# Performance work log

Hardware: AMD Instinct MI355X
Metric: run time of the kernel (lower is better)

## Reference

```python
import jax, jax.numpy as jnp
import numpy as np
from jax import lax

EPS_NORM = 1e-12   # F.normalize default eps
KS = 3             # fixed 3x3 window
K2 = KS * KS
MIN_CONN, MAX_CONN = 1, 8
NUM_GROUPS = 16    # largest divisor <=16 of C=128
GN_EPS = 1e-5


def _unfold3x3_reflect(x):
    # x: [B,C,H,W] -> patches [B,C,9,H,W] (reflect-padded 3x3 neighborhoods)
    B, C, H, W = x.shape
    p = jnp.pad(x, ((0, 0), (0, 0), (1, 1), (1, 1)), mode='reflect')
    pats = [p[:, :, dy:dy + H, dx:dx + W] for dy in range(KS) for dx in range(KS)]
    return jnp.stack(pats, axis=2)


def _df_counts(x):
    # DFDetector: mean over C, fixed Laplacian conv (zero pad), abs, per-batch min-max norm
    B = x.shape[0]
    avg = jnp.mean(x, axis=1, keepdims=True)  # [B,1,H,W]
    kern = jnp.array([[0., -1., 0.], [-1., 4., -1.], [0., -1., 0.]],
                     dtype=x.dtype).reshape(1, 1, 3, 3)
    df = jnp.abs(lax.conv_general_dilated(
        avg, kern, window_strides=(1, 1), padding=((1, 1), (1, 1)),
        dimension_numbers=('NCHW', 'OIHW', 'NCHW')))
    dmin = df.reshape(B, -1).min(axis=1).reshape(B, 1, 1, 1)
    dmax = df.reshape(B, -1).max(axis=1).reshape(B, 1, 1, 1)
    dn = (df - dmin) / (dmax - dmin + 1e-8)
    return MIN_CONN + jnp.round(dn * (MAX_CONN - MIN_CONN))  # [B,1,H,W], values in [1,8]


def _group_norm(x, w, b):
    B, C, H, W = x.shape
    g = x.reshape(B, NUM_GROUPS, -1)
    mu = g.mean(-1, keepdims=True)
    var = g.var(-1, keepdims=True)  # biased, matches torch GroupNorm
    g = (g - mu) * lax.rsqrt(var + GN_EPS)
    return g.reshape(B, C, H, W) * w[None, :, None, None] + b[None, :, None, None]


def setup_inputs() -> dict:
    key = jax.random.key(0)
    ks = jax.random.split(key, 7)
    B, C, H, W = 8, 128, 96, 96
    return {
        'x': jax.random.normal(ks[0], (B, C, H, W), jnp.float32),
        'gn_weight': jax.random.uniform(ks[1], (C,), jnp.float32, 0.5, 1.5),
        'gn_bias': jax.random.normal(ks[2], (C,), jnp.float32) * 0.1,
        'w1': jax.random.normal(ks[3], (2 * C, C), jnp.float32) * 0.02,
        'b1': jax.random.normal(ks[4], (2 * C,), jnp.float32) * 0.02,
        'w2': jax.random.normal(ks[5], (C, 2 * C), jnp.float32) * 0.02,
        'b2': jax.random.normal(ks[6], (C,), jnp.float32) * 0.02,
    }


def reference(x, gn_weight, gn_bias, w1, b1, w2, b2):
    B, C, H, W = x.shape
    P = H * W
    # per-pixel connection counts (integer k in [1,8]); non-differentiable in original
    counts = lax.stop_gradient(_df_counts(x))
    kvals = jnp.minimum(counts, K2).astype(jnp.int32).reshape(B, 1, P)

    patches = _unfold3x3_reflect(x).reshape(B, C, K2, P)
    xc = x.reshape(B, C, P)
    # L2 normalize over channel dim (F.normalize, eps=1e-12)
    cn = xc / jnp.maximum(jnp.linalg.norm(xc, axis=1, keepdims=True), EPS_NORM)
    pn = patches / jnp.maximum(jnp.linalg.norm(patches, axis=1, keepdims=True), EPS_NORM)

    sim = jnp.einsum('bcp,bckp->bkp', cn, pn)          # [B,9,P] cosine sims
    order = jnp.argsort(-sim, axis=1)                   # descending (== topk order)
    top_sim = jnp.take_along_axis(sim, order, axis=1)
    mask = jnp.arange(K2)[None, :, None] < kvals        # rank < k -> selected
    wts = jnp.exp(top_sim) * mask
    wts = wts / jnp.sum(wts, axis=1, keepdims=True)     # softmax over selected sims

    pat_sorted = jnp.take_along_axis(patches, order[:, None, :, :], axis=2)
    out = jnp.einsum('bckp,bkp->bcp', pat_sorted, wts).reshape(B, C, H, W)

    enhanced = out + _group_norm(x, gn_weight, gn_bias)
    h = jax.nn.relu(jnp.einsum('oi,bihw->bohw', w1, enhanced) + b1[None, :, None, None])
    ffn = jnp.einsum('oi,bihw->bohw', w2, h) + b2[None, :, None, None]
    return enhanced + ffn
```

## Files before the change

kernel.cpp:

```cpp
#include <hip/hip_runtime.h>

#define BD 8
#define CD 128
#define HD 96
#define WD 96
#define PD 9216
#define ND 73728

typedef __attribute__((ext_vector_type(8))) short short8;
typedef __attribute__((ext_vector_type(4))) float f32x4;

__device__ inline float bfu2f(unsigned int u) { return __uint_as_float(u << 16); }
__device__ inline unsigned short f2bfu(float f) {
  unsigned int u = __float_as_uint(f);
  u += 0x7fffu + ((u >> 16) & 1u);
  return (unsigned short)(u >> 16);
}

template<bool F32>
__device__ __forceinline__ float ldv(const void* __restrict__ p, size_t i) {
  if constexpr (F32) return ((const float*)p)[i];
  else return bfu2f(((const unsigned short*)p)[i]);
}

__global__ void k_init(unsigned long long* dmm, int* cnt) {
  int t = threadIdx.x;
  if (t < 8) dmm[t] = 0x7FEFFFFFFFFFFFFFULL;
  else if (t < 16) dmm[t] = 0ULL;
  if (t == 16) { cnt[0] = 0; cnt[1] = 0; }
}

__global__ void k_detect(const unsigned int* __restrict__ xw, int* __restrict__ cnt) {
  int t = blockIdx.x * 256 + threadIdx.x;
  uint4 w = ((const uint4*)xw)[t];
  int lz = (int)((w.x & 0xFFFFu) == 0u) + (int)((w.y & 0xFFFFu) == 0u) +
           (int)((w.z & 0xFFFFu) == 0u) + (int)((w.w & 0xFFFFu) == 0u);
  int e2 = (int)(((w.x >> 7) & 0xFFu) == 0xFFu) + (int)(((w.y >> 7) & 0xFFu) == 0xFFu) +
           (int)(((w.z >> 7) & 0xFFu) == 0xFFu) + (int)(((w.w >> 7) & 0xFFu) == 0xFFu);
  #pragma unroll
  for (int off = 32; off; off >>= 1) {
    lz += __shfl_down(lz, off);
    e2 += __shfl_down(e2, off);
  }
  if ((threadIdx.x & 63) == 0) { atomicAdd(&cnt[0], lz); atomicAdd(&cnt[1], e2); }
}

__global__ void k_flag(const int* __restrict__ cnt, int* __restrict__ flag) {
  *flag = (cnt[0] > 4096 || cnt[1] > 0) ? 1 : 0;
}

__global__ void k_cvtw(const void* __restrict__ w1, const void* __restrict__ w2,
                       unsigned short* __restrict__ wc, const int* __restrict__ flag) {
  bool f32 = (*flag != 0);
  int t = blockIdx.x * 256 + threadIdx.x;
  if (t < 32768)
    wc[t] = f32 ? f2bfu(((const float*)w1)[t]) : ((const unsigned short*)w1)[t];
  else {
    int u = t - 32768;
    wc[t] = f32 ? f2bfu(((const float*)w2)[u]) : ((const unsigned short*)w2)[u];
  }
}

__global__ void k_cvtb(const void* __restrict__ gw, const void* __restrict__ gb,
                       const void* __restrict__ b1, const void* __restrict__ b2,
                       float* __restrict__ prm, const int* __restrict__ flag) {
  bool f32 = (*flag != 0);
  int t = threadIdx.x;
  for (int i = t; i < 640; i += 256) {
    float v;
    if (i < 128)      v = f32 ? ((const float*)gw)[i]       : bfu2f(((const unsigned short*)gw)[i]);
    else if (i < 256) v = f32 ? ((const float*)gb)[i - 128] : bfu2f(((const unsigned short*)gb)[i - 128]);
    else if (i < 512) v = f32 ? ((const float*)b1)[i - 256] : bfu2f(((const unsigned short*)b1)[i - 256]);
    else              v = f32 ? ((const float*)b2)[i - 512] : bfu2f(((const unsigned short*)b2)[i - 512]);
    prm[i] = v;
  }
}

template<bool F32>
__device__ __forceinline__ void pmt_body(const void* __restrict__ x,
                                         float* __restrict__ xpm,
                                         double* __restrict__ avg, double* __restrict__ nrm,
                                         double* __restrict__ gpart,
                                         float (*tile)[132]) {
  const int t = threadIdx.x, px = t & 63, ci = t >> 6;
  const int gp0 = blockIdx.x * 64, b = gp0 / PD, p0 = gp0 - b * PD;
  double sg[4] = {0.0, 0.0, 0.0, 0.0}, qg[4] = {0.0, 0.0, 0.0, 0.0};
  for (int j = 0; j < 32; ++j) {
    int c = ci * 32 + j;
    float v = ldv<F32>(x, (size_t)(b * CD + c) * PD + p0 + px);
    tile[px][c] = v;
    sg[j >> 3] += (double)v;
    qg[j >> 3] += (double)v * (double)v;
  }
  #pragma unroll
  for (int g = 0; g < 4; ++g) {
    #pragma unroll
    for (int off = 32; off; off >>= 1) {
      sg[g] += __shfl_down(sg[g], off);
      qg[g] += __shfl_down(qg[g], off);
    }
  }
  if (px == 0) {
    double* gp_ = gpart + (size_t)blockIdx.x * 32;
    #pragma unroll
    for (int g = 0; g < 4; ++g) {
      gp_[(ci * 4 + g) * 2 + 0] = sg[g];
      gp_[(ci * 4 + g) * 2 + 1] = qg[g];
    }
  }
  __syncthreads();
  for (int i = t; i < 2048; i += 256) {
    int r = i >> 5, seg = i & 31;
    *(float4*)(xpm + (size_t)(gp0 + r) * 128 + seg * 4) = *(const float4*)&tile[r][seg * 4];
  }
  if (t < 64) {
    double s = 0.0, q = 0.0;
    for (int c = 0; c < 128; ++c) {
      float v = tile[t][c];
      s += (double)v;
      q += (double)v * (double)v;
    }
    avg[gp0 + t] = s * (1.0 / 128.0);
    nrm[gp0 + t] = sqrt(q);
  }
}
__global__ __launch_bounds__(256) void k_pmt(const void* __restrict__ x,
                                             const int* __restrict__ flag,
                                             float* __restrict__ xpm,
                                             double* __restrict__ avg,
                                             double* __restrict__ nrm,
                                             double* __restrict__ gpart) {
  __shared__ float tile[64][132];
  if (*flag) pmt_body<true>(x, xpm, avg, nrm, gpart, tile);
  else pmt_body<false>(x, xpm, avg, nrm, gpart, tile);
}

__global__ void k_gn2(const double* __restrict__ gpart, float* __restrict__ gn) {
  const int bg = blockIdx.x;
  const int b = bg >> 4, g = bg & 15;
  const int t = threadIdx.x;
  double s = 0.0, q = 0.0;
  for (int i = t; i < 144; i += 64) {
    const double* pp = gpart + (size_t)(b * 144 + i) * 32 + g * 2;
    s += pp[0];
    q += pp[1];
  }
  #pragma unroll
  for (int off = 32; off; off >>= 1) {
    s += __shfl_down(s, off);
    q += __shfl_down(q, off);
  }
  if (t == 0) {
    double mu = s / 73728.0;
    double var = q / 73728.0 - mu * mu;
    gn[bg] = (float)mu;
    gn[128 + bg] = (float)(1.0 / sqrt(var + 1e-5));
  }
}

__device__ inline double lap_df(const double* __restrict__ a, int b, int y, int x) {
  const double* ab = a + (size_t)b * PD;
  double v = 4.0 * ab[y * WD + x];
  if (y > 0)      v -= ab[(y - 1) * WD + x];
  if (y < HD - 1) v -= ab[(y + 1) * WD + x];
  if (x > 0)      v -= ab[y * WD + x - 1];
  if (x < WD - 1) v -= ab[y * WD + x + 1];
  return fabs(v);
}

__global__ void k_minmax(const double* __restrict__ avg, unsigned long long* __restrict__ dmm) {
  __shared__ double mnW[4], mxW[4];
  int t = threadIdx.x;
  int gp = blockIdx.x * 256 + t;
  int b = gp / PD, p = gp - b * PD;
  double mn = lap_df(avg, b, p / WD, p % WD);
  double mx = mn;
  #pragma unroll
  for (int off = 32; off; off >>= 1) {
    mn = fmin(mn, __shfl_down(mn, off));
    mx = fmax(mx, __shfl_down(mx, off));
  }
  if ((t & 63) == 0) { mnW[t >> 6] = mn; mxW[t >> 6] = mx; }
  __syncthreads();
  if (t == 0) {
    mn = fmin(fmin(mnW[0], mnW[1]), fmin(mnW[2], mnW[3]));
    mx = fmax(fmax(mxW[0], mxW[1]), fmax(mxW[2], mxW[3]));
    atomicMin(&dmm[b], (unsigned long long)__double_as_longlong(mn));
    atomicMax(&dmm[b + 8], (unsigned long long)__double_as_longlong(mx));
  }
}

__device__ __forceinline__ void neigh9(int y, int xx, int* q) {
  #pragma unroll
  for (int dy = 0; dy < 3; ++dy) {
    int yy = y + dy - 1;
    yy = yy < 0 ? -yy : (yy >= HD ? 2 * HD - 2 - yy : yy);
    #pragma unroll
    for (int dx = 0; dx < 3; ++dx) {
      int xr = xx + dx - 1;
      xr = xr < 0 ? -xr : (xr >= WD ? 2 * WD - 2 - xr : xr);
      q[dy * 3 + dx] = yy * WD + xr;
    }
  }
}

__global__ __launch_bounds__(256, 3) void k_ipg(const float* __restrict__ xpm,
                                                const double* __restrict__ avg,
                                                const double* __restrict__ nrm,
                                                const unsigned long long* __restrict__ dmm,
                                                const float* __restrict__ gn,
                                                const float* __restrict__ prm,
                                                unsigned short* __restrict__ eg) {
  __shared__ float tileF[12800];
  float4* tile4 = (float4*)tileF;
  const float* gwf = prm;
  const float* gbf = prm + 128;

  const int t = threadIdx.x;
  const int lb = (blockIdx.x & 7) * 144 + (blockIdx.x >> 3);
  const int b = lb / 144;
  const int tid = lb - b * 144;
  const int ty = tid / 12, tx = tid - ty * 12;
  const int y0 = ty * 8, x0 = tx * 8;

  {
    const int s = t & 31, hpb = t >> 5;
    #pragma unroll
    for (int it = 0; it < 13; ++it) {
      int hp = it * 8 + hpb;
      if (hp < 100) {
        int hr = hp / 10, hc = hp - hr * 10;
        int gy = y0 - 1 + hr; gy = gy < 0 ? -gy : (gy >= HD ? 2 * HD - 2 - gy : gy);
        int gx = x0 - 1 + hc; gx = gx < 0 ? -gx : (gx >= WD ? 2 * WD - 2 - gx : gx);
        const float4* src = (const float4*)(xpm + (size_t)(b * PD + gy * WD + gx) * 128) + s;
        tile4[(hp * 32 + s) ^ (hp & 7)] = *src;
      }
    }
  }
  __syncthreads();

  const int a = t >> 2, q = t & 3;
  const int yl = a >> 3, xl = a & 7;
  const int y = y0 + yl, xx = x0 + xl;
  const int p = y * WD + xx;
  const int cpix = (yl + 1) * 10 + (xl + 1);
  const int cub = cpix * 32 + q * 8, csw = cpix & 7;

  double sd[9];
  {
    float cv[32];
    #pragma unroll
    for (int j4 = 0; j4 < 8; ++j4)
      *(float4*)(cv + 4 * j4) = tile4[(cub + j4) ^ csw];
    #pragma unroll
    for (int k = 0; k < 9; ++k) {
      int dy = k / 3, dx = k - dy * 3;
      int pix = (yl + dy) * 10 + (xl + dx);
      int ub = pix * 32 + q * 8, sw = pix & 7;
      double acc = 0.0;
      #pragma unroll
      for (int seg = 0; seg < 8; ++seg) {
        float4 nv = tile4[(ub + seg) ^ sw];
        acc += (double)cv[seg * 4 + 0] * (double)nv.x;
        acc += (double)cv[seg * 4 + 1] * (double)nv.y;
        acc += (double)cv[seg * 4 + 2] * (double)nv.z;
        acc += (double)cv[seg * 4 + 3] * (double)nv.w;
      }
      double v1 = __shfl_down(acc, 1);
      double v2 = __shfl_down(acc, 2);
      double v3 = __shfl_down(acc, 3);
      sd[k] = ((acc + v1) + v2) + v3;
    }
  }

  float wv[9];
  #pragma unroll
  for (int j = 0; j < 9; ++j) wv[j] = 0.f;
  if (q == 0) {
    int qg[9];
    neigh9(y, xx, qg);
    double dmin = __longlong_as_double((long long)dmm[b]);
    double dmax = __longlong_as_double((long long)dmm[b + 8]);
    double df = lap_df(avg, b, y, xx);
    double dn = (df - dmin) / (dmax - dmin + 1e-8);
    int kk = 1 + (int)rint(dn * 7.0);
    kk = kk < 1 ? 1 : (kk > 8 ? 8 : kk);

    double np_ = fmax(nrm[b * PD + p], 1e-12);
    #pragma unroll
    for (int k = 0; k < 9; ++k) {
      double nq = fmax(nrm[b * PD + qg[k]], 1e-12);
      sd[k] = sd[k] / (np_ * nq);
    }
    float w[9];
    float wsum = 0.f;
    #pragma unroll
    for (int j = 0; j < 9; ++j) {
      int rank = 0;
      #pragma unroll
      for (int i = 0; i < 9; ++i)
        rank += (sd[i] > sd[j]) || (sd[i] == sd[j] && i < j);
      w[j] = (rank < kk) ? expf((float)sd[j]) : 0.f;
      wsum += w[j];
    }
    float inv = 1.f / wsum;
    #pragma unroll
    for (int j = 0; j < 9; ++j) wv[j] = w[j] * inv;
  }
  #pragma unroll
  for (int j = 0; j < 9; ++j) wv[j] = __shfl(wv[j], (t & 63) & ~3);

  {
    float og[32];
    #pragma unroll
    for (int j = 0; j < 32; ++j) og[j] = 0.f;
    #pragma unroll
    for (int k = 0; k < 9; ++k) {
      int dy = k / 3, dx = k - dy * 3;
      int pix = (yl + dy) * 10 + (xl + dx);
      int ub = pix * 32 + q * 8, sw = pix & 7;
      #pragma unroll
      for (int seg = 0; seg < 8; ++seg) {
        float4 nv = tile4[(ub + seg) ^ sw];
        og[seg * 4 + 0] += wv[k] * nv.x;
        og[seg * 4 + 1] += wv[k] * nv.y;
        og[seg * 4 + 2] += wv[k] * nv.z;
        og[seg * 4 + 3] += wv[k] * nv.w;
      }
    }
    const int g16 = b * 16;
    unsigned short* egr = eg + (size_t)(b * PD + p) * 128 + q * 32;
    #pragma unroll
    for (int seg = 0; seg < 4; ++seg) {
      float4 cA = tile4[(cub + seg * 2) ^ csw];
      float4 cB = tile4[(cub + seg * 2 + 1) ^ csw];
      float cvv[8] = {cA.x, cA.y, cA.z, cA.w, cB.x, cB.y, cB.z, cB.w};
      int g = q * 4 + seg;
      float mu = gn[g16 + g], rs = gn[128 + g16 + g];
      unsigned int pkd[4];
      #pragma unroll
      for (int j = 0; j < 8; ++j) {
        int c = q * 32 + seg * 8 + j;
        float e = og[seg * 8 + j] + (cvv[j] - mu) * rs * gwf[c] + gbf[c];
        unsigned int h = (unsigned int)f2bfu(e);
        if (j & 1) pkd[j >> 1] |= h << 16;
        else pkd[j >> 1] = h;
      }
      uint4 v; v.x = pkd[0]; v.y = pkd[1]; v.z = pkd[2]; v.w = pkd[3];
      *(uint4*)(egr + seg * 8) = v;
    }
  }
}

__global__ __launch_bounds__(256, 3) void k_ffn(const unsigned short* __restrict__ eg,
                                                const float* __restrict__ prm,
                                                const unsigned short* __restrict__ wc,
                                                float* __restrict__ outp) {
  __shared__ unsigned short et[64][136];
  __shared__ unsigned short Hl[64][264];
  const float* b1f = prm + 256;
  const float* b2f = prm + 512;

  const int t = threadIdx.x;
  const int lb = (blockIdx.x & 7) * 144 + (blockIdx.x >> 3);
  const int gp0 = lb * 64;
  const int b = gp0 / PD, p0b = gp0 - b * PD;

  const unsigned short* wc1 = wc;
  const unsigned short* wc2 = wc + 32768;
  const int lane = t & 63, wave = t >> 6;
  const int r16 = lane & 15, quad = lane >> 4;

  {
    const uint4* eg4 = (const uint4*)(eg + (size_t)gp0 * 128);
    #pragma unroll
    for (int it = 0; it < 4; ++it) {
      int lin = it * 256 + t;
      int row = lin >> 4, c8 = lin & 15;
      *(uint4*)&et[row][c8 * 8] = eg4[lin];
    }
  }
  short8 wb1[16];
  #pragma unroll
  for (int kk = 0; kk < 4; ++kk)
    #pragma unroll
    for (int nt = 0; nt < 4; ++nt)
      wb1[kk * 4 + nt] = *(const short8*)(wc1 + (size_t)(wave * 64 + nt * 16 + r16) * 128 + kk * 32 + quad * 8);
  __syncthreads();

  f32x4 acc[16];
  #pragma unroll
  for (int i = 0; i < 16; ++i) acc[i] = (f32x4){0.f, 0.f, 0.f, 0.f};
  #pragma unroll
  for (int kk = 0; kk < 4; ++kk) {
    short8 afm[4];
    #pragma unroll
    for (int m = 0; m < 4; ++m)
      afm[m] = *(const short8*)&et[m * 16 + r16][kk * 32 + quad * 8];
    #pragma unroll
    for (int nt = 0; nt < 4; ++nt)
      #pragma unroll
      for (int m = 0; m < 4; ++m)
        acc[m * 4 + nt] = __builtin_amdgcn_mfma_f32_16x16x32_bf16(afm[m], wb1[kk * 4 + nt], acc[m * 4 + nt], 0, 0, 0);
  }
  #pragma unroll
  for (int nt = 0; nt < 4; ++nt) {
    int n = wave * 64 + nt * 16 + r16;
    float bias = b1f[n];
    #pragma unroll
    for (int m = 0; m < 4; ++m)
      #pragma unroll
      for (int r = 0; r < 4; ++r)
        Hl[m * 16 + quad * 4 + r][n] = f2bfu(fmaxf(acc[m * 4 + nt][r] + bias, 0.f));
  }
  short8 wb2[16];
  #pragma unroll
  for (int kk = 0; kk < 8; ++kk)
    #pragma unroll
    for (int nt = 0; nt < 2; ++nt)
      wb2[kk * 2 + nt] = *(const short8*)(wc2 + (size_t)(wave * 32 + nt * 16 + r16) * 256 + kk * 32 + quad * 8);
  __syncthreads();

  f32x4 acc2[8];
  #pragma unroll
  for (int i = 0; i < 8; ++i) acc2[i] = (f32x4){0.f, 0.f, 0.f, 0.f};
  #pragma unroll
  for (int kk = 0; kk < 8; ++kk) {
    short8 afm[4];
    #pragma unroll
    for (int m = 0; m < 4; ++m)
      afm[m] = *(const short8*)&Hl[m * 16 + r16][kk * 32 + quad * 8];
    #pragma unroll
    for (int nt = 0; nt < 2; ++nt)
      #pragma unroll
      for (int m = 0; m < 4; ++m)
        acc2[m * 2 + nt] = __builtin_amdgcn_mfma_f32_16x16x32_bf16(afm[m], wb2[kk * 2 + nt], acc2[m * 2 + nt], 0, 0, 0);
  }
  #pragma unroll
  for (int nt = 0; nt < 2; ++nt) {
    int n = wave * 32 + nt * 16 + r16;
    float bias = b2f[n];
    #pragma unroll
    for (int m = 0; m < 4; ++m) {
      int mloc0 = m * 16 + quad * 4;
      float4 o;
      o.x = acc2[m * 2 + nt][0] + bias + bfu2f(et[mloc0 + 0][n]);
      o.y = acc2[m * 2 + nt][1] + bias + bfu2f(et[mloc0 + 1][n]);
      o.z = acc2[m * 2 + nt][2] + bias + bfu2f(et[mloc0 + 2][n]);
      o.w = acc2[m * 2 + nt][3] + bias + bfu2f(et[mloc0 + 3][n]);
      *(float4*)(outp + (size_t)(b * CD + n) * PD + p0b + mloc0) = o;
    }
  }
}

extern "C" void kernel_launch(void* const* d_in, const int* in_sizes, int n_in,
                              void* d_out, int out_size, void* d_ws, size_t ws_size,
                              hipStream_t stream) {
  const void* x  = d_in[0];
  const void* gw = d_in[1];
  const void* gb = d_in[2];
  const void* w1 = d_in[3];
  const void* b1 = d_in[4];
  const void* w2 = d_in[5];
  const void* b2 = d_in[6];
  float* out = (float*)d_out;

  char* ws = (char*)d_ws;
  int* flag = (int*)ws;
  int* cnt = (int*)(ws + 16);
  unsigned long long* dmm = (unsigned long long*)(ws + 128);
  float* gn = (float*)(ws + 256);
  float* prm = (float*)(ws + 1280);
  unsigned short* wc = (unsigned short*)(ws + 3840);
  double* avg = (double*)(ws + 134912);
  double* nrm = (double*)(ws + 724736);
  double* gpart = (double*)(ws + 1314560);
  unsigned short* eg = (unsigned short*)(ws + 1609472);
  float* xpm = (float*)(ws + 20483840);

  k_init<<<1, 64, 0, stream>>>(dmm, cnt);
  k_detect<<<64, 256, 0, stream>>>((const unsigned int*)x, cnt);
  k_flag<<<1, 1, 0, stream>>>(cnt, flag);
  k_cvtw<<<256, 256, 0, stream>>>(w1, w2, wc, flag);
  k_cvtb<<<1, 256, 0, stream>>>(gw, gb, b1, b2, prm, flag);
  k_pmt<<<ND / 64, 256, 0, stream>>>(x, flag, xpm, avg, nrm, gpart);
  k_gn2<<<128, 64, 0, stream>>>(gpart, gn);
  k_minmax<<<ND / 256, 256, 0, stream>>>(avg, dmm);
  k_ipg<<<ND / 64, 256, 0, stream>>>(xpm, avg, nrm, dmm, gn, prm, eg);
  k_ffn<<<ND / 64, 256, 0, stream>>>(eg, prm, wc, out);
}
```

Before: 192.2 us.

## Exploit cosine-similarity symmetry to halve neighbor dot products in k_ipg

Because the dot product between a pixel and its neighbor is symmetric, k_ipg now computes only the four 'upper' neighbor dots per pixel. It fetches the other four from adjacent pixels through a small shared-memory array, and computes them directly only at tile edges. The self-dot comes from a new nrm2 buffer precomputed in k_pmt. This roughly halves the fp64 dot-product work, at the cost of an extra block barrier, divergent tile-edge paths and an extra workspace buffer. Separately, k_pmt and k_minmax remap block indices so consecutive blocks interleave across batches, aiming at better locality across the chip's partitions.

```diff
diff --git a/kernel.cpp b/kernel.cpp
--- a/kernel.cpp
+++ b/kernel.cpp
@@ -80,10 +80,11 @@
 __device__ __forceinline__ void pmt_body(const void* __restrict__ x,
                                          float* __restrict__ xpm,
                                          double* __restrict__ avg, double* __restrict__ nrm,
+                                         double* __restrict__ nrm2,
                                          double* __restrict__ gpart,
-                                         float (*tile)[132]) {
+                                         float (*tile)[132], int lb) {
   const int t = threadIdx.x, px = t & 63, ci = t >> 6;
-  const int gp0 = blockIdx.x * 64, b = gp0 / PD, p0 = gp0 - b * PD;
+  const int gp0 = lb * 64, b = gp0 / PD, p0 = gp0 - b * PD;
   double sg[4] = {0.0, 0.0, 0.0, 0.0}, qg[4] = {0.0, 0.0, 0.0, 0.0};
   for (int j = 0; j < 32; ++j) {
     int c = ci * 32 + j;
@@ -101,7 +102,7 @@
     }
   }
   if (px == 0) {
-    double* gp_ = gpart + (size_t)blockIdx.x * 32;
+    double* gp_ = gpart + (size_t)lb * 32;
     #pragma unroll
     for (int g = 0; g < 4; ++g) {
       gp_[(ci * 4 + g) * 2 + 0] = sg[g];
@@ -120,8 +121,16 @@
       s += (double)v;
       q += (double)v * (double)v;
     }
+    double qq[4] = {0.0, 0.0, 0.0, 0.0};
+    #pragma unroll
+    for (int g = 0; g < 4; ++g)
+      for (int i = 0; i < 32; ++i) {
+        float v = tile[t][g * 32 + i];
+        qq[g] += (double)v * (double)v;
+      }
     avg[gp0 + t] = s * (1.0 / 128.0);
     nrm[gp0 + t] = sqrt(q);
+    nrm2[gp0 + t] = ((qq[0] + qq[1]) + qq[2]) + qq[3];
   }
 }
 __global__ __launch_bounds__(256) void k_pmt(const void* __restrict__ x,
@@ -129,10 +138,12 @@
                                              float* __restrict__ xpm,
                                              double* __restrict__ avg,
                                              double* __restrict__ nrm,
+                                             double* __restrict__ nrm2,
                                              double* __restrict__ gpart) {
   __shared__ float tile[64][132];
-  if (*flag) pmt_body<true>(x, xpm, avg, nrm, gpart, tile);
-  else pmt_body<false>(x, xpm, avg, nrm, gpart, tile);
+  const int lb = (blockIdx.x & 7) * 144 + (blockIdx.x >> 3);
+  if (*flag) pmt_body<true>(x, xpm, avg, nrm, nrm2, gpart, tile, lb);
+  else pmt_body<false>(x, xpm, avg, nrm, nrm2, gpart, tile, lb);
 }
 
 __global__ void k_gn2(const double* __restrict__ gpart, float* __restrict__ gn) {
@@ -171,7 +182,8 @@
 __global__ void k_minmax(const double* __restrict__ avg, unsigned long long* __restrict__ dmm) {
   __shared__ double mnW[4], mxW[4];
   int t = threadIdx.x;
-  int gp = blockIdx.x * 256 + t;
+  const int lb = (blockIdx.x & 7) * 36 + (blockIdx.x >> 3);
+  int gp = lb * 256 + t;
   int b = gp / PD, p = gp - b * PD;
   double mn = lap_df(avg, b, p / WD, p % WD);
   double mx = mn;
@@ -207,11 +219,13 @@
 __global__ __launch_bounds__(256, 3) void k_ipg(const float* __restrict__ xpm,
                                                 const double* __restrict__ avg,
                                                 const double* __restrict__ nrm,
+                                                const double* __restrict__ nrm2,
                                                 const unsigned long long* __restrict__ dmm,
                                                 const float* __restrict__ gn,
                                                 const float* __restrict__ prm,
                                                 unsigned short* __restrict__ eg) {
   __shared__ float tileF[12800];
+  __shared__ double sdl[64][4];
   float4* tile4 = (float4*)tileF;
   const float* gwf = prm;
   const float* gbf = prm + 128;
@@ -246,7 +260,12 @@
   const int cpix = (yl + 1) * 10 + (xl + 1);
   const int cub = cpix * 32 + q * 8, csw = cpix & 7;
 
-  double sd[9];
+  const bool nb5 = (xl == 7);
+  const bool nb6 = (yl == 7) || (xl == 0);
+  const bool nb7 = (yl == 7);
+  const bool nb8 = (yl == 7) || (xl == 7);
+
+  double d[9];
   {
     float cv[32];
     #pragma unroll
@@ -254,24 +273,32 @@
       *(float4*)(cv + 4 * j4) = tile4[(cub + j4) ^ csw];
     #pragma unroll
     for (int k = 0; k < 9; ++k) {
-      int dy = k / 3, dx = k - dy * 3;
-      int pix = (yl + dy) * 10 + (xl + dx);
-      int ub = pix * 32 + q * 8, sw = pix & 7;
-      double acc = 0.0;
-      #pragma unroll
-      for (int seg = 0; seg < 8; ++seg) {
-        float4 nv = tile4[(ub + seg) ^ sw];
-        acc += (double)cv[seg * 4 + 0] * (double)nv.x;
-        acc += (double)cv[seg * 4 + 1] * (double)nv.y;
-        acc += (double)cv[seg * 4 + 2] * (double)nv.z;
-        acc += (double)cv[seg * 4 + 3] * (double)nv.w;
+      if (k == 4) continue;
+      bool need = (k < 4) || (k == 5 ? nb5 : k == 6 ? nb6 : k == 7 ? nb7 : nb8);
+      if (need) {
+        int dy = k / 3, dx = k - dy * 3;
+        int pix = (yl + dy) * 10 + (xl + dx);
+        int ub = pix * 32 + q * 8, sw = pix & 7;
+        double acc = 0.0;
+        #pragma unroll
+        for (int seg = 0; seg < 8; ++seg) {
+          float4 nv = tile4[(ub + seg) ^ sw];
+          acc += (double)cv[seg * 4 + 0] * (double)nv.x;
+          acc += (double)cv[seg * 4 + 1] * (double)nv.y;
+          acc += (double)cv[seg * 4 + 2] * (double)nv.z;
+          acc += (double)cv[seg * 4 + 3] * (double)nv.w;
+        }
+        double v1 = __shfl_down(acc, 1);
+        double v2 = __shfl_down(acc, 2);
+        double v3 = __shfl_down(acc, 3);
+        d[k] = ((acc + v1) + v2) + v3;
       }
-      double v1 = __shfl_down(acc, 1);
-      double v2 = __shfl_down(acc, 2);
-      double v3 = __shfl_down(acc, 3);
-      sd[k] = ((acc + v1) + v2) + v3;
-    }
-  }
+    }
+  }
+  if (q == 0) {
+    sdl[a][0] = d[0]; sdl[a][1] = d[1]; sdl[a][2] = d[2]; sdl[a][3] = d[3];
+  }
+  __syncthreads();
 
   float wv[9];
   #pragma unroll
@@ -285,6 +312,14 @@
     double dn = (df - dmin) / (dmax - dmin + 1e-8);
     int kk = 1 + (int)rint(dn * 7.0);
     kk = kk < 1 ? 1 : (kk > 8 ? 8 : kk);
+
+    double sd[9];
+    sd[0] = d[0]; sd[1] = d[1]; sd[2] = d[2]; sd[3] = d[3];
+    sd[4] = nrm2[b * PD + p];
+    sd[5] = nb5 ? d[5] : sdl[a + 1][3];
+    sd[6] = nb6 ? d[6] : sdl[a + 7][2];
+    sd[7] = nb7 ? d[7] : sdl[a + 8][1];
+    sd[8] = nb8 ? d[8] : sdl[a + 9][0];
 
     double np_ = fmax(nrm[b * PD + p], 1e-12);
     #pragma unroll
@@ -474,18 +509,19 @@
   unsigned short* wc = (unsigned short*)(ws + 3840);
   double* avg = (double*)(ws + 134912);
   double* nrm = (double*)(ws + 724736);
-  double* gpart = (double*)(ws + 1314560);
-  unsigned short* eg = (unsigned short*)(ws + 1609472);
-  float* xpm = (float*)(ws + 20483840);
+  double* nrm2 = (double*)(ws + 1314560);
+  double* gpart = (double*)(ws + 1904384);
+  unsigned short* eg = (unsigned short*)(ws + 2199296);
+  float* xpm = (float*)(ws + 21073664);
 
   k_init<<<1, 64, 0, stream>>>(dmm, cnt);
   k_detect<<<64, 256, 0, stream>>>((const unsigned int*)x, cnt);
   k_flag<<<1, 1, 0, stream>>>(cnt, flag);
   k_cvtw<<<256, 256, 0, stream>>>(w1, w2, wc, flag);
   k_cvtb<<<1, 256, 0, stream>>>(gw, gb, b1, b2, prm, flag);
-  k_pmt<<<ND / 64, 256, 0, stream>>>(x, flag, xpm, avg, nrm, gpart);
+  k_pmt<<<ND / 64, 256, 0, stream>>>(x, flag, xpm, avg, nrm, nrm2, gpart);
   k_gn2<<<128, 64, 0, stream>>>(gpart, gn);
   k_minmax<<<ND / 256, 256, 0, stream>>>(avg, dmm);
-  k_ipg<<<ND / 64, 256, 0, stream>>>(xpm, avg, nrm, dmm, gn, prm, eg);
+  k_ipg<<<ND / 64, 256, 0, stream>>>(xpm, avg, nrm, nrm2, dmm, gn, prm, eg);
   k_ffn<<<ND / 64, 256, 0, stream>>>(eg, prm, wc, out);
 }
```

Measured after the change: 192.2 us. No clear change (+0.0%).
